# Kernel tuning notes

Hardware: AMD Instinct MI355X
Metric: run time of the kernel (lower is better)

The kernel has to match this reference:

```python
import jax, jax.numpy as jnp
import numpy as np

ALIGN_CORNERS = True   # module init arg
NUM_AUX = 8            # auxiliary samples for linearized multi-sampling
NOISE_STRENGTH = 0.5   # noise scale in units of input pixel spacing
EPS = 1e-6             # Tikhonov term for the per-pixel 2x2 least squares


def _base_coords(n, align_corners):
    if align_corners:
        return jnp.linspace(-1.0, 1.0, n, dtype=jnp.float32)
    return (jnp.arange(n, dtype=jnp.float32) * 2.0 + 1.0) / n - 1.0


def affine_grid(theta, h_out, w_out, align_corners):
    # theta: [B,2,3] -> grid [B,h_out,w_out,2] with (x,y) in [-1,1]
    xs = _base_coords(w_out, align_corners)
    ys = _base_coords(h_out, align_corners)
    X, Y = jnp.meshgrid(xs, ys)                      # [H,W]
    base = jnp.stack([X, Y, jnp.ones_like(X)], -1)   # [H,W,3]
    return jnp.einsum('hwk,bik->bhwi', base, theta)  # [B,H,W,2]


def bilinear_sample(image, grid, align_corners):
    # image [B,C,Hi,Wi], grid [B,H,W,2] -> [B,H,W,C], zero padding outside
    B, C, Hi, Wi = image.shape
    x, y = grid[..., 0], grid[..., 1]
    if align_corners:
        ix = (x + 1.0) * 0.5 * (Wi - 1)
        iy = (y + 1.0) * 0.5 * (Hi - 1)
    else:
        ix = ((x + 1.0) * Wi - 1.0) * 0.5
        iy = ((y + 1.0) * Hi - 1.0) * 0.5
    x0 = jnp.floor(ix); y0 = jnp.floor(iy)
    wx1 = ix - x0; wy1 = iy - y0
    bidx = jnp.arange(B)[:, None, None]

    def tap(xi, yi, w):
        valid = (xi >= 0) & (xi <= Wi - 1) & (yi >= 0) & (yi <= Hi - 1)
        xc = jnp.clip(xi, 0, Wi - 1).astype(jnp.int32)
        yc = jnp.clip(yi, 0, Hi - 1).astype(jnp.int32)
        v = image[bidx, :, yc, xc]                   # [B,H,W,C] gather
        return v * (w * valid)[..., None]

    return (tap(x0, y0, (1 - wx1) * (1 - wy1)) +
            tap(x0 + 1, y0, wx1 * (1 - wy1)) +
            tap(x0, y0 + 1, (1 - wx1) * wy1) +
            tap(x0 + 1, y0 + 1, wx1 * wy1))


def linearized_grid_sample(image, grid, align_corners):
    # Linearized multi-sampling (Jiang et al., ICCV'19): forward value equals
    # the center bilinear sample; gradient wrt grid flows through a per-pixel
    # least-squares linearization fitted from NUM_AUX noisy auxiliary samples.
    B, C, Hi, Wi = image.shape
    key = jax.random.key(42)
    spacing = jnp.array([2.0 / Wi, 2.0 / Hi], dtype=jnp.float32)  # one input pixel in norm coords
    g0 = jax.lax.stop_gradient(grid)
    noise = jax.random.normal(key, (B, NUM_AUX) + grid.shape[1:3] + (2,), dtype=jnp.float32)
    aux = g0[:, None] + noise * NOISE_STRENGTH * spacing          # [B,K,H,W,2]

    center = bilinear_sample(image, g0, align_corners)            # [B,H,W,C]
    samp = jax.vmap(lambda g: bilinear_sample(image, g, align_corners),
                    in_axes=1, out_axes=1)(aux)                   # [B,K,H,W,C]

    d_int = samp - center[:, None]                                # [B,K,H,W,C]
    d_grid = aux - g0[:, None]                                    # [B,K,H,W,2]
    xtx = jnp.einsum('bkhwi,bkhwj->bhwij', d_grid, d_grid) \
        + EPS * jnp.eye(2, dtype=jnp.float32)                     # [B,H,W,2,2]
    xty = jnp.einsum('bkhwi,bkhwc->bhwic', d_grid, d_int)         # [B,H,W,2,C]
    slope = jnp.linalg.solve(xtx, xty)                            # [B,H,W,2,C]

    out = center + jnp.einsum('bhwic,bhwi->bhwc', slope, grid - g0)
    return jnp.transpose(out, (0, 3, 1, 2))                       # [B,C,H,W]


def setup_inputs() -> dict:
    key = jax.random.key(0)
    k1, k2 = jax.random.split(key)
    B, C, Hi, Wi = 4, 3, 1024, 1024
    image = jax.random.normal(k1, (B, C, Hi, Wi), dtype=jnp.float32)
    ident = jnp.tile(jnp.array([[1.0, 0.0, 0.0], [0.0, 1.0, 0.0]], dtype=jnp.float32), (B, 1, 1))
    pMtrx = ident + 0.05 * jax.random.normal(k2, (B, 2, 3), dtype=jnp.float32)
    return {"image": image, "pMtrx": pMtrx, "W": 1024, "H": 1024}


def reference(image, pMtrx, W, H):
    # torch.affine_grid_generator(pMtrx, (B,3,W,H)) -> grid [B, W, H, 2]
    grid = affine_grid(pMtrx, W, H, ALIGN_CORNERS)
    return linearized_grid_sample(image, grid, ALIGN_CORNERS)  # [B,C,W,H]
```

## Files before the change

### kernel.cpp

```cpp
#include <hip/hip_runtime.h>


#define B_  4
#define C_  3
#define HI  1024
#define WI  1024
#define HO  1024
#define WO  1024

__global__ __launch_bounds__(256) void warp_bilinear_kernel(
    const float* __restrict__ image,
    const float* __restrict__ theta,
    float* __restrict__ out)
{
    const int idx = blockIdx.x * blockDim.x + threadIdx.x;
    const int w = idx & (WO - 1);
    const int h = (idx >> 10) & (HO - 1);
    const int b = idx >> 20;

    const float xs = -1.0f + 2.0f * (float)w / (float)(WO - 1);
    const float ys = -1.0f + 2.0f * (float)h / (float)(HO - 1);

    const float* t = theta + b * 6;
    const float x = t[0] * xs + t[1] * ys + t[2];
    const float y = t[3] * xs + t[4] * ys + t[5];

    const float ix = (x + 1.0f) * 0.5f * (float)(WI - 1);
    const float iy = (y + 1.0f) * 0.5f * (float)(HI - 1);

    const float x0f = floorf(ix);
    const float y0f = floorf(iy);
    const float wx1 = ix - x0f;
    const float wy1 = iy - y0f;
    const float wx0 = 1.0f - wx1;
    const float wy0 = 1.0f - wy1;

    const int x0 = (int)x0f;
    const int y0 = (int)y0f;
    const int x1 = x0 + 1;
    const int y1 = y0 + 1;

    const bool vx0 = (x0 >= 0) && (x0 <= WI - 1);
    const bool vx1 = (x1 >= 0) && (x1 <= WI - 1);
    const bool vy0 = (y0 >= 0) && (y0 <= HI - 1);
    const bool vy1 = (y1 >= 0) && (y1 <= HI - 1);

    const int xc0 = min(max(x0, 0), WI - 1);
    const int xc1 = min(max(x1, 0), WI - 1);
    const int yc0 = min(max(y0, 0), HI - 1);
    const int yc1 = min(max(y1, 0), HI - 1);

    const float w00 = wx0 * wy0 * ((vx0 && vy0) ? 1.0f : 0.0f);
    const float w10 = wx1 * wy0 * ((vx1 && vy0) ? 1.0f : 0.0f);
    const float w01 = wx0 * wy1 * ((vx0 && vy1) ? 1.0f : 0.0f);
    const float w11 = wx1 * wy1 * ((vx1 && vy1) ? 1.0f : 0.0f);

    const int o00 = yc0 * WI + xc0;
    const int o10 = yc0 * WI + xc1;
    const int o01 = yc1 * WI + xc0;
    const int o11 = yc1 * WI + xc1;

    const float* imgb = image + (size_t)b * (C_ * HI * WI);
    float* ob = out + (size_t)b * (C_ * HO * WO) + h * WO + w;

#pragma unroll
    for (int c = 0; c < C_; ++c) {
        const float* p = imgb + c * (HI * WI);
        const float v = p[o00] * w00 + p[o10] * w10 + p[o01] * w01 + p[o11] * w11;
        ob[c * (HO * WO)] = v;
    }
}

extern "C" void kernel_launch(void* const* d_in, const int* in_sizes, int n_in,
                              void* d_out, int out_size, void* d_ws, size_t ws_size,
                              hipStream_t stream) {
    const float* image = (const float*)d_in[0];
    const float* theta = (const float*)d_in[1];
    float* out = (float*)d_out;

    const int total = B_ * HO * WO;
    const int block = 256;
    const int grid = total / block;
    warp_bilinear_kernel<<<grid, block, 0, stream>>>(image, theta, out);
}
```

Before: 118.4 us.

## Process four pixels per thread with paired-tap loads and vectorized nontemporal stores

Each thread now handles four consecutive output pixels of one row. The row-dependent affine terms are hoisted, and each bilinear row pair is fetched as one packed two-float load with select logic for edge clamping. Outputs are written as 16-byte nontemporal vector stores. The aim is fewer load and store instructions and better write efficiency, at the cost of unaligned 8-byte loads and fewer threads in flight.

```diff
diff --git a/kernel.cpp b/kernel.cpp
--- a/kernel.cpp
+++ b/kernel.cpp
@@ -8,66 +8,82 @@
 #define HO  1024
 #define WO  1024
 
-__global__ __launch_bounds__(256) void warp_bilinear_kernel(
+typedef float vf4 __attribute__((ext_vector_type(4)));
+struct __attribute__((packed)) fpair { float a, b; };
+
+__global__ __launch_bounds__(256) void warp_bilinear4_kernel(
     const float* __restrict__ image,
     const float* __restrict__ theta,
     float* __restrict__ out)
 {
-    const int idx = blockIdx.x * blockDim.x + threadIdx.x;
-    const int w = idx & (WO - 1);
-    const int h = (idx >> 10) & (HO - 1);
-    const int b = idx >> 20;
-
-    const float xs = -1.0f + 2.0f * (float)w / (float)(WO - 1);
-    const float ys = -1.0f + 2.0f * (float)h / (float)(HO - 1);
+    const int h = blockIdx.x & (HO - 1);
+    const int b = blockIdx.x >> 10;
+    const int w0 = threadIdx.x << 2;
 
     const float* t = theta + b * 6;
-    const float x = t[0] * xs + t[1] * ys + t[2];
-    const float y = t[3] * xs + t[4] * ys + t[5];
+    const float t0 = t[0], t1 = t[1], t2 = t[2];
+    const float t3 = t[3], t4 = t[4], t5 = t[5];
 
-    const float ix = (x + 1.0f) * 0.5f * (float)(WI - 1);
-    const float iy = (y + 1.0f) * 0.5f * (float)(HI - 1);
-
-    const float x0f = floorf(ix);
-    const float y0f = floorf(iy);
-    const float wx1 = ix - x0f;
-    const float wy1 = iy - y0f;
-    const float wx0 = 1.0f - wx1;
-    const float wy0 = 1.0f - wy1;
-
-    const int x0 = (int)x0f;
-    const int y0 = (int)y0f;
-    const int x1 = x0 + 1;
-    const int y1 = y0 + 1;
-
-    const bool vx0 = (x0 >= 0) && (x0 <= WI - 1);
-    const bool vx1 = (x1 >= 0) && (x1 <= WI - 1);
-    const bool vy0 = (y0 >= 0) && (y0 <= HI - 1);
-    const bool vy1 = (y1 >= 0) && (y1 <= HI - 1);
-
-    const int xc0 = min(max(x0, 0), WI - 1);
-    const int xc1 = min(max(x1, 0), WI - 1);
-    const int yc0 = min(max(y0, 0), HI - 1);
-    const int yc1 = min(max(y1, 0), HI - 1);
-
-    const float w00 = wx0 * wy0 * ((vx0 && vy0) ? 1.0f : 0.0f);
-    const float w10 = wx1 * wy0 * ((vx1 && vy0) ? 1.0f : 0.0f);
-    const float w01 = wx0 * wy1 * ((vx0 && vy1) ? 1.0f : 0.0f);
-    const float w11 = wx1 * wy1 * ((vx1 && vy1) ? 1.0f : 0.0f);
-
-    const int o00 = yc0 * WI + xc0;
-    const int o10 = yc0 * WI + xc1;
-    const int o01 = yc1 * WI + xc0;
-    const int o11 = yc1 * WI + xc1;
+    const float ys = -1.0f + 2.0f * (float)h / (float)(HO - 1);
+    const float cy = t1 * ys + t2;
+    const float dy = t4 * ys + t5;
 
     const float* imgb = image + (size_t)b * (C_ * HI * WI);
-    float* ob = out + (size_t)b * (C_ * HO * WO) + h * WO + w;
+    float acc[C_][4];
 
 #pragma unroll
+    for (int px = 0; px < 4; ++px) {
+        const int w = w0 + px;
+        const float xs = -1.0f + 2.0f * (float)w / (float)(WO - 1);
+        const float x = t0 * xs + cy;
+        const float y = t3 * xs + dy;
+
+        const float ix = (x + 1.0f) * 0.5f * (float)(WI - 1);
+        const float iy = (y + 1.0f) * 0.5f * (float)(HI - 1);
+
+        const float x0f = floorf(ix);
+        const float y0f = floorf(iy);
+        const float wx1 = ix - x0f;
+        const float wy1 = iy - y0f;
+
+        const int x0 = (int)x0f;
+        const int y0 = (int)y0f;
+
+        const float ax0 = (1.0f - wx1) * ((x0 >= 0 && x0 <= WI - 1) ? 1.0f : 0.0f);
+        const float ax1 = wx1          * ((x0 >= -1 && x0 <= WI - 2) ? 1.0f : 0.0f);
+        const float ay0 = (1.0f - wy1) * ((y0 >= 0 && y0 <= HI - 1) ? 1.0f : 0.0f);
+        const float ay1 = wy1          * ((y0 >= -1 && y0 <= HI - 2) ? 1.0f : 0.0f);
+
+        const int xb  = min(max(x0, 0), WI - 2);
+        const int xc0 = min(max(x0, 0), WI - 1);
+        const int xc1 = min(max(x0 + 1, 0), WI - 1);
+        const bool s0 = (xc0 != xb);
+        const bool s1 = (xc1 == xb);
+
+        const int yc0 = min(max(y0, 0), HI - 1);
+        const int yc1 = min(max(y0 + 1, 0), HI - 1);
+        const int o0 = yc0 * WI + xb;
+        const int o1 = yc1 * WI + xb;
+
+#pragma unroll
+        for (int c = 0; c < C_; ++c) {
+            const float* p = imgb + c * (HI * WI);
+            const fpair p0 = *(const fpair*)(p + o0);
+            const fpair p1 = *(const fpair*)(p + o1);
+            const float va0 = s0 ? p0.b : p0.a;
+            const float vb0 = s1 ? p0.a : p0.b;
+            const float va1 = s0 ? p1.b : p1.a;
+            const float vb1 = s1 ? p1.a : p1.b;
+            acc[c][px] = ay0 * (ax0 * va0 + ax1 * vb0)
+                       + ay1 * (ax0 * va1 + ax1 * vb1);
+        }
+    }
+
+    float* ob = out + (size_t)b * (C_ * HO * WO) + h * WO + w0;
+#pragma unroll
     for (int c = 0; c < C_; ++c) {
-        const float* p = imgb + c * (HI * WI);
-        const float v = p[o00] * w00 + p[o10] * w10 + p[o01] * w01 + p[o11] * w11;
-        ob[c * (HO * WO)] = v;
+        vf4 v = { acc[c][0], acc[c][1], acc[c][2], acc[c][3] };
+        __builtin_nontemporal_store(v, (vf4*)(ob + c * (HO * WO)));
     }
 }
 
@@ -78,8 +94,6 @@
     const float* theta = (const float*)d_in[1];
     float* out = (float*)d_out;
 
-    const int total = B_ * HO * WO;
-    const int block = 256;
-    const int grid = total / block;
-    warp_bilinear_kernel<<<grid, block, 0, stream>>>(image, theta, out);
+    const int grid = B_ * HO;
+    warp_bilinear4_kernel<<<grid, 256, 0, stream>>>(image, theta, out);
 }
```

Measured after the change: 122.8 us. 3.7% more time.
